# Optimization experiments

Measured on AMD Instinct MI355X. Metric: run time of the kernel, lower is better.

Reference implementation:

```python
import jax, jax.numpy as jnp
import numpy as np


def setup_inputs() -> dict:
    key = jax.random.key(0)
    k_idx, k_val = jax.random.split(key)
    XSIZE = 128
    N = 500000
    B = 16
    indices = jax.random.randint(k_idx, (N, 3), 0, XSIZE, dtype=jnp.int32)
    values = jax.random.normal(k_val, (B, N), dtype=jnp.float32)
    return {"indices": indices, "values": values, "xsize": XSIZE}


def reference(indices, values, xsize):
    # densitySmoothnessVolume: scatter-add values into a (B, X, X, X) grid,
    # then TV and MSE smoothness losses over 3-axis finite differences.
    B = values.shape[0]
    X = xsize
    # flat voxel index (z, y, x) -> z*X*X + y*X + x ; shared across batch
    flat = (indices[:, 0].astype(jnp.int32) * X + indices[:, 1]) * X + indices[:, 2]
    grid = jnp.zeros((B, X * X * X), dtype=values.dtype)
    grid = grid.at[:, flat].add(values)  # scatter-add, duplicate indices accumulate
    grid = grid.reshape(B, X, X, X)

    d1 = grid[:, 1:, :, :] - grid[:, :-1, :, :]
    d2 = grid[:, :, 1:, :] - grid[:, :, :-1, :]
    d3 = grid[:, :, :, 1:] - grid[:, :, :, :-1]

    axes = (1, 2, 3)
    # total variation loss, normalized by number of voxels X^3
    num_pixels = jnp.asarray(X * X * X, dtype=values.dtype)
    tv = (jnp.sum(jnp.abs(d1), axis=axes)
          + jnp.sum(jnp.abs(d2), axis=axes)
          + jnp.sum(jnp.abs(d3), axis=axes)) / num_pixels

    # MSE smoothness loss; normalizer replicates TF code exactly:
    # 2 * prod(shape[1:3]) - shape[1] - shape[2] = 2*X^2 - 2*X
    num_pixel_pairs = jnp.asarray(2 * X * X - 2 * X, dtype=values.dtype)
    mse = (jnp.sum(jnp.square(d1), axis=axes)
           + jnp.sum(jnp.square(d2), axis=axes)
           + jnp.sum(jnp.square(d3), axis=axes)) / num_pixel_pairs

    return jnp.stack([tv, mse])  # [2, B]
```

## Files before the change

### kernel.cpp

```cpp
#include <hip/hip_runtime.h>

#define XS 128
#define PLANE (XS * XS)
#define X3 (XS * XS * XS)
#define ZC 8
#define RCHUNK 2048

__global__ __launch_bounds__(256) void hist_kernel(
    const int* __restrict__ idx, int* __restrict__ hist, int N)
{
    __shared__ int lh[XS];
    for (int i = threadIdx.x; i < XS; i += blockDim.x) lh[i] = 0;
    __syncthreads();
    for (int n = blockIdx.x * blockDim.x + threadIdx.x; n < N;
         n += gridDim.x * blockDim.x)
        atomicAdd(&lh[idx[3 * n]], 1);
    __syncthreads();
    for (int i = threadIdx.x; i < XS; i += blockDim.x)
        if (lh[i]) atomicAdd(&hist[i], lh[i]);
}

__global__ void scan_kernel(const int* __restrict__ hist,
                            int* __restrict__ base, int* __restrict__ cursor)
{
    if (threadIdx.x == 0) {
        int acc = 0;
        for (int i = 0; i < XS; ++i) {
            base[i] = acc; cursor[i] = acc; acc += hist[i];
        }
    }
}

__global__ __launch_bounds__(256) void reorder_kernel(
    const int* __restrict__ idx, int* __restrict__ cursor,
    int2* __restrict__ list, int N)
{
    __shared__ int lh[XS], lbase[XS];
    const int c0 = blockIdx.x * RCHUNK;
    const int c1 = (c0 + RCHUNK < N) ? c0 + RCHUNK : N;

    for (int i = threadIdx.x; i < XS; i += blockDim.x) lh[i] = 0;
    __syncthreads();
    for (int n = c0 + threadIdx.x; n < c1; n += blockDim.x)
        atomicAdd(&lh[idx[3 * n]], 1);
    __syncthreads();
    for (int i = threadIdx.x; i < XS; i += blockDim.x) {
        lbase[i] = lh[i] ? atomicAdd(&cursor[i], lh[i]) : 0;
        lh[i] = 0;
    }
    __syncthreads();
    for (int n = c0 + threadIdx.x; n < c1; n += blockDim.x) {
        const int z = idx[3 * n], y = idx[3 * n + 1], x = idx[3 * n + 2];
        const int r = atomicAdd(&lh[z], 1);
        list[lbase[z] + r] = make_int2(n, (y << 7) | x);
    }
}

__global__ __launch_bounds__(1024, 4) void fused_kernel(
    const int2* __restrict__ list, const int* __restrict__ base,
    const int* __restrict__ cnt, const float* __restrict__ vals,
    float* __restrict__ out,
    int N, int Btot)
{
    __shared__ float buf[2][PLANE];
    __shared__ float rtv[16], rms[16];

    const int b    = blockIdx.x;
    const int z0   = blockIdx.y * ZC;
    const int tid  = threadIdx.x;
    const float* vb = vals + (size_t)b * N;

    float tv = 0.f, ms = 0.f;

    for (int i = tid; i < PLANE; i += 1024) buf[0][i] = 0.f;
    __syncthreads();
    {
        const int s0 = base[z0], c = cnt[z0];
        int e = tid;
        for (; e + 3072 < c; e += 4096) {
            int2 e0 = list[s0 + e], e1 = list[s0 + e + 1024];
            int2 e2 = list[s0 + e + 2048], e3 = list[s0 + e + 3072];
            float v0 = vb[e0.x], v1 = vb[e1.x], v2 = vb[e2.x], v3 = vb[e3.x];
            atomicAdd(&buf[0][e0.y], v0); atomicAdd(&buf[0][e1.y], v1);
            atomicAdd(&buf[0][e2.y], v2); atomicAdd(&buf[0][e3.y], v3);
        }
        for (; e < c; e += 1024) {
            int2 en = list[s0 + e];
            atomicAdd(&buf[0][en.y], vb[en.x]);
        }
    }
    __syncthreads();

    for (int k = 1; k <= ZC; ++k) {
        float* cur = buf[(k - 1) & 1];
        float* nxt = buf[k & 1];
        const int z = z0 + k;
        const bool haveNext = (z < XS);

        if (haveNext) {
            for (int i = tid; i < PLANE; i += 1024) nxt[i] = 0.f;
        }
        __syncthreads();
        if (haveNext) {
            const int s0 = base[z], c = cnt[z];
            int e = tid;
            for (; e + 3072 < c; e += 4096) {
                int2 e0 = list[s0 + e], e1 = list[s0 + e + 1024];
                int2 e2 = list[s0 + e + 2048], e3 = list[s0 + e + 3072];
                float v0 = vb[e0.x], v1 = vb[e1.x], v2 = vb[e2.x], v3 = vb[e3.x];
                atomicAdd(&nxt[e0.y], v0); atomicAdd(&nxt[e1.y], v1);
                atomicAdd(&nxt[e2.y], v2); atomicAdd(&nxt[e3.y], v3);
            }
            for (; e < c; e += 1024) {
                int2 en = list[s0 + e];
                atomicAdd(&nxt[en.y], vb[en.x]);
            }
        }
        __syncthreads();

        const float4* c4 = (const float4*)cur;
        const float4* n4 = (const float4*)nxt;
        for (int q = tid; q < PLANE / 4; q += 1024) {
            const int qx = q & 31;
            const int y  = q >> 5;
            const float4 a = c4[q];
            float d;
            d = a.y - a.x; tv += fabsf(d); ms += d * d;
            d = a.z - a.y; tv += fabsf(d); ms += d * d;
            d = a.w - a.z; tv += fabsf(d); ms += d * d;
            if (qx < 31) {
                d = cur[4 * q + 4] - a.w; tv += fabsf(d); ms += d * d;
            }
            if (y < XS - 1) {
                const float4 u = c4[q + 32];
                d = u.x - a.x; tv += fabsf(d); ms += d * d;
                d = u.y - a.y; tv += fabsf(d); ms += d * d;
                d = u.z - a.z; tv += fabsf(d); ms += d * d;
                d = u.w - a.w; tv += fabsf(d); ms += d * d;
            }
            if (haveNext) {
                const float4 u = n4[q];
                d = u.x - a.x; tv += fabsf(d); ms += d * d;
                d = u.y - a.y; tv += fabsf(d); ms += d * d;
                d = u.z - a.z; tv += fabsf(d); ms += d * d;
                d = u.w - a.w; tv += fabsf(d); ms += d * d;
            }
        }
        __syncthreads();
    }

    for (int o = 32; o > 0; o >>= 1) {
        tv += __shfl_down(tv, o); ms += __shfl_down(ms, o);
    }
    if ((tid & 63) == 0) { rtv[tid >> 6] = tv; rms[tid >> 6] = ms; }
    __syncthreads();
    if (tid == 0) {
        float t = 0.f, m = 0.f;
        #pragma unroll
        for (int w = 0; w < 16; ++w) { t += rtv[w]; m += rms[w]; }
        atomicAdd(out + b,        t * (1.0f / (float)X3));
        atomicAdd(out + Btot + b, m * (1.0f / (float)(2 * XS * XS - 2 * XS)));
    }
}

extern "C" void kernel_launch(void* const* d_in, const int* in_sizes, int n_in,
                              void* d_out, int out_size, void* d_ws, size_t ws_size,
                              hipStream_t stream)
{
    const int*   indices = (const int*)d_in[0];
    const float* values  = (const float*)d_in[1];
    const int N = in_sizes[0] / 3;
    const int B = in_sizes[1] / N;
    float* out = (float*)d_out;
    char*  ws  = (char*)d_ws;

    int2* list   = (int2*)ws;
    int*  hist   = (int*)(ws + (size_t)N * sizeof(int2));
    int*  basep  = hist + XS;
    int*  cursor = basep + XS;

    hipMemsetAsync(d_out, 0, (size_t)out_size * sizeof(float), stream);
    hipMemsetAsync(hist, 0, XS * sizeof(int), stream);

    hist_kernel<<<256, 256, 0, stream>>>(indices, hist, N);
    scan_kernel<<<1, 64, 0, stream>>>(hist, basep, cursor);
    reorder_kernel<<<(N + RCHUNK - 1) / RCHUNK, 256, 0, stream>>>(
        indices, cursor, list, N);
    fused_kernel<<<dim3(B, XS / ZC), 1024, 0, stream>>>(
        list, basep, hist, values, out, N, B);
}
```

Before: 176.3 us.

## Restructure pipeline: single-buffer fused kernel with register prefetch, vectorized index loads, parallel scan

The fused kernel now keeps one 64KB shared plane instead of two, carries the previous plane in registers for the z-difference, and prefetches the next plane's list entries and gathered values into registers while the current plane is processed. Block size drops to 512 threads and z-chunk to 4, giving more blocks and less shared memory per block. Index loads in hist and reorder use int4 vector loads, the scan becomes a parallel Hillis-Steele scan that also zeroes the output (removing one memset), and custom barriers wait only on LDS counters. The risks are more register pressure from the prefetch and carried-plane arrays, and more redundant boundary-plane scatter work from the smaller z-chunk.

```diff
diff --git a/kernel.cpp b/kernel.cpp
--- a/kernel.cpp
+++ b/kernel.cpp
@@ -3,32 +3,57 @@
 #define XS 128
 #define PLANE (XS * XS)
 #define X3 (XS * XS * XS)
-#define ZC 8
-#define RCHUNK 2048
+#define ZC 4
+#define TPB 512
+#define SLOTS 8
+#define QPT 8
+
+__device__ __forceinline__ void bar_lgkm() {
+    __builtin_amdgcn_sched_barrier(0);
+    asm volatile("s_waitcnt lgkmcnt(0)" ::: "memory");
+    __builtin_amdgcn_s_barrier();
+    __builtin_amdgcn_sched_barrier(0);
+}
 
 __global__ __launch_bounds__(256) void hist_kernel(
     const int* __restrict__ idx, int* __restrict__ hist, int N)
 {
     __shared__ int lh[XS];
-    for (int i = threadIdx.x; i < XS; i += blockDim.x) lh[i] = 0;
-    __syncthreads();
-    for (int n = blockIdx.x * blockDim.x + threadIdx.x; n < N;
-         n += gridDim.x * blockDim.x)
+    for (int i = threadIdx.x; i < XS; i += 256) lh[i] = 0;
+    __syncthreads();
+    const int n4 = N >> 2;
+    const int4* p = (const int4*)idx;
+    for (int g = blockIdx.x * 256 + threadIdx.x; g < n4; g += gridDim.x * 256) {
+        int4 A = p[3 * g], B = p[3 * g + 1], C = p[3 * g + 2];
+        atomicAdd(&lh[A.x], 1); atomicAdd(&lh[A.w], 1);
+        atomicAdd(&lh[B.z], 1); atomicAdd(&lh[C.y], 1);
+    }
+    for (int n = (n4 << 2) + blockIdx.x * 256 + threadIdx.x; n < N;
+         n += gridDim.x * 256)
         atomicAdd(&lh[idx[3 * n]], 1);
     __syncthreads();
-    for (int i = threadIdx.x; i < XS; i += blockDim.x)
+    for (int i = threadIdx.x; i < XS; i += 256)
         if (lh[i]) atomicAdd(&hist[i], lh[i]);
 }
 
-__global__ void scan_kernel(const int* __restrict__ hist,
-                            int* __restrict__ base, int* __restrict__ cursor)
-{
-    if (threadIdx.x == 0) {
-        int acc = 0;
-        for (int i = 0; i < XS; ++i) {
-            base[i] = acc; cursor[i] = acc; acc += hist[i];
-        }
-    }
+__global__ __launch_bounds__(128) void scan_kernel(
+    const int* __restrict__ hist, int* __restrict__ base,
+    int* __restrict__ cursor, float* __restrict__ out, int osz)
+{
+    __shared__ int sh[XS];
+    const int t = threadIdx.x;
+    const int h = hist[t];
+    sh[t] = h;
+    __syncthreads();
+    for (int o = 1; o < XS; o <<= 1) {
+        int v = (t >= o) ? sh[t - o] : 0;
+        __syncthreads();
+        sh[t] += v;
+        __syncthreads();
+    }
+    const int excl = sh[t] - h;
+    base[t] = excl; cursor[t] = excl;
+    if (t < osz) out[t] = 0.f;
 }
 
 __global__ __launch_bounds__(256) void reorder_kernel(
@@ -36,117 +61,154 @@
     int2* __restrict__ list, int N)
 {
     __shared__ int lh[XS], lbase[XS];
-    const int c0 = blockIdx.x * RCHUNK;
-    const int c1 = (c0 + RCHUNK < N) ? c0 + RCHUNK : N;
-
-    for (int i = threadIdx.x; i < XS; i += blockDim.x) lh[i] = 0;
-    __syncthreads();
-    for (int n = c0 + threadIdx.x; n < c1; n += blockDim.x)
-        atomicAdd(&lh[idx[3 * n]], 1);
-    __syncthreads();
-    for (int i = threadIdx.x; i < XS; i += blockDim.x) {
+    const int c0 = blockIdx.x * 1024;
+    int z[4], key[4], nn[4];
+    int cntm = 0;
+
+    for (int i = threadIdx.x; i < XS; i += 256) lh[i] = 0;
+
+    if (c0 + 1024 <= N) {
+        const int t = threadIdx.x;
+        const int4* p = (const int4*)(idx + (size_t)c0 * 3);
+        int4 A = p[3 * t], B = p[3 * t + 1], C = p[3 * t + 2];
+        const int nb = c0 + 4 * t;
+        z[0] = A.x; key[0] = (A.y << 7) | A.z; nn[0] = nb;
+        z[1] = A.w; key[1] = (B.x << 7) | B.y; nn[1] = nb + 1;
+        z[2] = B.z; key[2] = (B.w << 7) | C.x; nn[2] = nb + 2;
+        z[3] = C.y; key[3] = (C.z << 7) | C.w; nn[3] = nb + 3;
+        cntm = 4;
+    } else {
+        #pragma unroll
+        for (int i = 0; i < 4; ++i) {
+            const int n = c0 + 4 * threadIdx.x + i;
+            if (n < N) {
+                z[cntm]   = idx[3 * n];
+                key[cntm] = (idx[3 * n + 1] << 7) | idx[3 * n + 2];
+                nn[cntm]  = n;
+                ++cntm;
+            }
+        }
+    }
+    __syncthreads();
+    #pragma unroll
+    for (int i = 0; i < 4; ++i)
+        if (i < cntm) atomicAdd(&lh[z[i]], 1);
+    __syncthreads();
+    for (int i = threadIdx.x; i < XS; i += 256) {
         lbase[i] = lh[i] ? atomicAdd(&cursor[i], lh[i]) : 0;
         lh[i] = 0;
     }
     __syncthreads();
-    for (int n = c0 + threadIdx.x; n < c1; n += blockDim.x) {
-        const int z = idx[3 * n], y = idx[3 * n + 1], x = idx[3 * n + 2];
-        const int r = atomicAdd(&lh[z], 1);
-        list[lbase[z] + r] = make_int2(n, (y << 7) | x);
-    }
-}
-
-__global__ __launch_bounds__(1024, 4) void fused_kernel(
+    #pragma unroll
+    for (int i = 0; i < 4; ++i)
+        if (i < cntm) {
+            const int r = atomicAdd(&lh[z[i]], 1);
+            list[lbase[z[i]] + r] = make_int2(nn[i], key[i]);
+        }
+}
+
+__global__ __launch_bounds__(TPB, 4) void fused_kernel(
     const int2* __restrict__ list, const int* __restrict__ base,
     const int* __restrict__ cnt, const float* __restrict__ vals,
-    float* __restrict__ out,
-    int N, int Btot)
-{
-    __shared__ float buf[2][PLANE];
-    __shared__ float rtv[16], rms[16];
-
-    const int b    = blockIdx.x;
-    const int z0   = blockIdx.y * ZC;
-    const int tid  = threadIdx.x;
+    float* __restrict__ out, int N, int Btot)
+{
+    __shared__ float buf[PLANE];
+    __shared__ float rtv[TPB / 64], rms[TPB / 64];
+
+    const int b   = blockIdx.x;
+    const int z0  = blockIdx.y * ZC;
+    const int tid = threadIdx.x;
     const float* vb = vals + (size_t)b * N;
-
+    const int pmax = (z0 + ZC < XS) ? (z0 + ZC) : (XS - 1);
+
+    int pos[SLOTS]; float val[SLOTS];
+    int pc = 0, ps0 = 0;
+
+    auto prefetch = [&](int zp) {
+        ps0 = base[zp]; pc = cnt[zp];
+        int2 e[SLOTS];
+        #pragma unroll
+        for (int i = 0; i < SLOTS; ++i) {
+            const int ix = ps0 + tid + i * TPB;
+            e[i] = list[ix < N ? ix : N - 1];
+        }
+        #pragma unroll
+        for (int i = 0; i < SLOTS; ++i) { pos[i] = e[i].y; val[i] = vb[e[i].x]; }
+    };
+    auto scatter = [&]() {
+        #pragma unroll
+        for (int i = 0; i < SLOTS; ++i) {
+            const float v = (tid + i * TPB < pc) ? val[i] : 0.f;
+            atomicAdd(&buf[pos[i]], v);
+        }
+        for (int e = SLOTS * TPB + tid; e < pc; e += TPB) {
+            const int2 en = list[ps0 + e];
+            atomicAdd(&buf[en.y], vb[en.x]);
+        }
+    };
+
+    prefetch(z0);
+    #pragma unroll
+    for (int i = 0; i < QPT; ++i)
+        ((float4*)buf)[tid + i * TPB] = make_float4(0.f, 0.f, 0.f, 0.f);
+    bar_lgkm();
+    scatter();
+    prefetch(z0 + 1);
+    bar_lgkm();
+
+    float4 prev[QPT];
     float tv = 0.f, ms = 0.f;
 
-    for (int i = tid; i < PLANE; i += 1024) buf[0][i] = 0.f;
-    __syncthreads();
-    {
-        const int s0 = base[z0], c = cnt[z0];
-        int e = tid;
-        for (; e + 3072 < c; e += 4096) {
-            int2 e0 = list[s0 + e], e1 = list[s0 + e + 1024];
-            int2 e2 = list[s0 + e + 2048], e3 = list[s0 + e + 3072];
-            float v0 = vb[e0.x], v1 = vb[e1.x], v2 = vb[e2.x], v3 = vb[e3.x];
-            atomicAdd(&buf[0][e0.y], v0); atomicAdd(&buf[0][e1.y], v1);
-            atomicAdd(&buf[0][e2.y], v2); atomicAdd(&buf[0][e3.y], v3);
-        }
-        for (; e < c; e += 1024) {
-            int2 en = list[s0 + e];
-            atomicAdd(&buf[0][en.y], vb[en.x]);
-        }
-    }
-    __syncthreads();
-
-    for (int k = 1; k <= ZC; ++k) {
-        float* cur = buf[(k - 1) & 1];
-        float* nxt = buf[k & 1];
-        const int z = z0 + k;
-        const bool haveNext = (z < XS);
-
-        if (haveNext) {
-            for (int i = tid; i < PLANE; i += 1024) nxt[i] = 0.f;
-        }
-        __syncthreads();
-        if (haveNext) {
-            const int s0 = base[z], c = cnt[z];
-            int e = tid;
-            for (; e + 3072 < c; e += 4096) {
-                int2 e0 = list[s0 + e], e1 = list[s0 + e + 1024];
-                int2 e2 = list[s0 + e + 2048], e3 = list[s0 + e + 3072];
-                float v0 = vb[e0.x], v1 = vb[e1.x], v2 = vb[e2.x], v3 = vb[e3.x];
-                atomicAdd(&nxt[e0.y], v0); atomicAdd(&nxt[e1.y], v1);
-                atomicAdd(&nxt[e2.y], v2); atomicAdd(&nxt[e3.y], v3);
+    for (int p = z0; p <= pmax; ++p) {
+        float4 a[QPT];
+        #pragma unroll
+        for (int i = 0; i < QPT; ++i)
+            a[i] = ((const float4*)buf)[tid + i * TPB];
+
+        if (p > z0) {
+            #pragma unroll
+            for (int i = 0; i < QPT; ++i) {
+                float d;
+                d = a[i].x - prev[i].x; tv += fabsf(d); ms += d * d;
+                d = a[i].y - prev[i].y; tv += fabsf(d); ms += d * d;
+                d = a[i].z - prev[i].z; tv += fabsf(d); ms += d * d;
+                d = a[i].w - prev[i].w; tv += fabsf(d); ms += d * d;
             }
-            for (; e < c; e += 1024) {
-                int2 en = list[s0 + e];
-                atomicAdd(&nxt[en.y], vb[en.x]);
+        }
+        if (p < z0 + ZC) {
+            #pragma unroll
+            for (int i = 0; i < QPT; ++i) {
+                const int q = tid + i * TPB;
+                const int qx = q & 31, y = q >> 5;
+                float d;
+                d = a[i].y - a[i].x; tv += fabsf(d); ms += d * d;
+                d = a[i].z - a[i].y; tv += fabsf(d); ms += d * d;
+                d = a[i].w - a[i].z; tv += fabsf(d); ms += d * d;
+                if (qx < 31) {
+                    d = buf[4 * q + 4] - a[i].w; tv += fabsf(d); ms += d * d;
+                }
+                if (y < XS - 1) {
+                    const float4 u = ((const float4*)buf)[q + 32];
+                    d = u.x - a[i].x; tv += fabsf(d); ms += d * d;
+                    d = u.y - a[i].y; tv += fabsf(d); ms += d * d;
+                    d = u.z - a[i].z; tv += fabsf(d); ms += d * d;
+                    d = u.w - a[i].w; tv += fabsf(d); ms += d * d;
+                }
             }
         }
-        __syncthreads();
-
-        const float4* c4 = (const float4*)cur;
-        const float4* n4 = (const float4*)nxt;
-        for (int q = tid; q < PLANE / 4; q += 1024) {
-            const int qx = q & 31;
-            const int y  = q >> 5;
-            const float4 a = c4[q];
-            float d;
-            d = a.y - a.x; tv += fabsf(d); ms += d * d;
-            d = a.z - a.y; tv += fabsf(d); ms += d * d;
-            d = a.w - a.z; tv += fabsf(d); ms += d * d;
-            if (qx < 31) {
-                d = cur[4 * q + 4] - a.w; tv += fabsf(d); ms += d * d;
-            }
-            if (y < XS - 1) {
-                const float4 u = c4[q + 32];
-                d = u.x - a.x; tv += fabsf(d); ms += d * d;
-                d = u.y - a.y; tv += fabsf(d); ms += d * d;
-                d = u.z - a.z; tv += fabsf(d); ms += d * d;
-                d = u.w - a.w; tv += fabsf(d); ms += d * d;
-            }
-            if (haveNext) {
-                const float4 u = n4[q];
-                d = u.x - a.x; tv += fabsf(d); ms += d * d;
-                d = u.y - a.y; tv += fabsf(d); ms += d * d;
-                d = u.z - a.z; tv += fabsf(d); ms += d * d;
-                d = u.w - a.w; tv += fabsf(d); ms += d * d;
-            }
-        }
-        __syncthreads();
+        #pragma unroll
+        for (int i = 0; i < QPT; ++i) prev[i] = a[i];
+
+        if (p < pmax) {
+            bar_lgkm();
+            #pragma unroll
+            for (int i = 0; i < QPT; ++i)
+                ((float4*)buf)[tid + i * TPB] = make_float4(0.f, 0.f, 0.f, 0.f);
+            bar_lgkm();
+            scatter();
+            if (p + 2 <= pmax) prefetch(p + 2);
+            bar_lgkm();
+        }
     }
 
     for (int o = 32; o > 0; o >>= 1) {
@@ -157,7 +219,7 @@
     if (tid == 0) {
         float t = 0.f, m = 0.f;
         #pragma unroll
-        for (int w = 0; w < 16; ++w) { t += rtv[w]; m += rms[w]; }
+        for (int w = 0; w < TPB / 64; ++w) { t += rtv[w]; m += rms[w]; }
         atomicAdd(out + b,        t * (1.0f / (float)X3));
         atomicAdd(out + Btot + b, m * (1.0f / (float)(2 * XS * XS - 2 * XS)));
     }
@@ -179,13 +241,11 @@
     int*  basep  = hist + XS;
     int*  cursor = basep + XS;
 
-    hipMemsetAsync(d_out, 0, (size_t)out_size * sizeof(float), stream);
     hipMemsetAsync(hist, 0, XS * sizeof(int), stream);
-
     hist_kernel<<<256, 256, 0, stream>>>(indices, hist, N);
-    scan_kernel<<<1, 64, 0, stream>>>(hist, basep, cursor);
-    reorder_kernel<<<(N + RCHUNK - 1) / RCHUNK, 256, 0, stream>>>(
+    scan_kernel<<<1, 128, 0, stream>>>(hist, basep, cursor, out, out_size);
+    reorder_kernel<<<(N + 1023) / 1024, 256, 0, stream>>>(
         indices, cursor, list, N);
-    fused_kernel<<<dim3(B, XS / ZC), 1024, 0, stream>>>(
+    fused_kernel<<<dim3(B, XS / ZC), TPB, 0, stream>>>(
         list, basep, hist, values, out, N, B);
 }
```

New measurement: 177.3 us. Within noise of the previous version (+0.6%).
